# Performance work log

Hardware: AMD Instinct MI355X
Metric: run time of the kernel (lower is better)

The kernel has to match this reference:

```python
import jax, jax.numpy as jnp
import numpy as np

B, D, C = 4096, 2048, 64
L_HP, D_HP, OMEGA, EPSILON = 0.5, 1.0, 100.0, 0.1
LN_EPS = 1e-5
CLASS_COUNTS = [5000,4500,4050,3645,3280,2952,2657,2391,2152,1937,1743,1569,1412,1271,1144,1029,926,834,750,675,608,547,492,443,399,359,323,291,262,236,212,191,172,155,139,125,113,101,91,82,74,66,60,54,48,43,39,35,32,28,26,23,21,19,17,15,14,12,11,10,9,8,7,7]


def setup_inputs() -> dict:
    key = jax.random.key(0)
    k_x, k_y, k_b, k_u1, k_u2 = jax.random.split(key, 5)
    counts = jnp.asarray(CLASS_COUNTS, dtype=jnp.float32)
    # set_class_weights: tilde_C = 1/log(counts*d + eps), min-max normalized, scaled by l
    tilde = 1.0 / jnp.log(counts * D_HP + EPSILON)
    c = (tilde - jnp.min(tilde)) / (jnp.max(tilde) - jnp.min(tilde)) * L_HP
    # set_fs_classes: 1 where count <= omega
    fs_classes = jnp.where(counts <= OMEGA, 1, 0).astype(jnp.int32)
    x = jax.random.normal(k_x, (B, D), dtype=jnp.float32)
    y = jax.random.randint(k_y, (B,), 0, C)
    beta_idx = jax.random.randint(k_b, (B,), 0, B)
    u1 = jax.random.uniform(k_u1, (B,))
    u2 = jax.random.uniform(k_u2, (B,))
    alpha = jnp.where(u1 > 0.5, u2, jnp.ones((B,), jnp.float32))
    return {"x": x, "y": y, "alpha": alpha, "beta_idx": beta_idx, "c": c, "fs_classes": fs_classes}


def reference(x, y, alpha, beta_idx, c, fs_classes):
    n_batch, dim = x.shape
    num_classes = c.shape[0]
    # --- reconstruct ---
    mu = jnp.mean(x, axis=-1, keepdims=True)
    var = jnp.mean((x - mu) ** 2, axis=-1, keepdims=True)
    x_norm = (x - mu) / jnp.sqrt(var + LN_EPS) / jnp.sqrt(jnp.asarray(dim, x.dtype))
    sim = jnp.matmul(x_norm, x_norm.T)  # [B, B]
    # E[i, j] = eye[i, j] + fs_mask[j]  (broadcast over rows), thresholded to {0, 1}
    fs_mask = fs_classes[y].astype(x.dtype)  # [B]
    E = jnp.eye(n_batch, dtype=x.dtype) + fs_mask[None, :]
    E = jnp.where(E >= 1.0, 1.0, 0.0)
    sim = jax.nn.softmax(sim - 100000.0 * E, axis=-1)
    contrib = c[y]  # [B]
    reconstructions = jnp.matmul(sim, x)  # [B, D]
    R = reconstructions * contrib[:, None] + x * (1.0 - contrib)[:, None]
    # --- pairwise_mix: M @ R with M[i,:] = alpha[i]*e_i + (1-alpha[i])*e_{beta_idx[i]} ---
    y_oh = jax.nn.one_hot(y, num_classes, dtype=x.dtype)
    a = alpha[:, None]
    x_mix = a * R + (1.0 - a) * R[beta_idx]
    y_mix = a * y_oh + (1.0 - a) * y_oh[beta_idx]
    return (x_mix, y_mix)
```

## Files before the change

### kernel.cpp

```cpp
#include <hip/hip_runtime.h>
#include <cstdint>
#include <cstddef>

typedef __bf16 bf16;
typedef __bf16 bf16x8 __attribute__((ext_vector_type(8)));
typedef float floatx4 __attribute__((ext_vector_type(4)));
typedef int intx8 __attribute__((ext_vector_type(8)));

#define NB 4096
#define ND 2048
#define NCLS 64
#define TSTRIDE 144
#define OS 136

__device__ __forceinline__ void stage16(const void* g, void* l) {
  __builtin_amdgcn_global_load_lds(
      (__attribute__((address_space(1))) unsigned int*)g,
      (__attribute__((address_space(3))) unsigned int*)l, 16, 0, 0);
}

__device__ __forceinline__ unsigned char fp8x1(float f) {
  return (unsigned char)(__builtin_amdgcn_cvt_pk_fp8_f32(f, f, 0, false) & 0xFF);
}
__device__ __forceinline__ int fp8x4(float f0, float f1, float f2, float f3) {
  int d = __builtin_amdgcn_cvt_pk_fp8_f32(f0, f1, 0, false);
  return __builtin_amdgcn_cvt_pk_fp8_f32(f2, f3, d, true);
}

__device__ __forceinline__ void stage_step(const unsigned char* __restrict__ A,
                                           const unsigned char* __restrict__ B,
                                           int K, int m0, int n0, int k0,
                                           unsigned char* As,
                                           unsigned char* Bs) {
  const int t = threadIdx.x;
  const int w = t >> 6, lane = t & 63;
#pragma unroll
  for (int q = 0; q < 4; ++q) {
    const int slot = w * 256 + q * 64 + lane;
    const int row = slot >> 3;
    const int cc = (slot & 7) ^ (row & 7);
    stage16(A + (size_t)(m0 + row) * K + (k0 + cc * 16),
            As + (w * 256 + q * 64) * 16);
  }
#pragma unroll
  for (int q = 0; q < 4; ++q) {
    const int slot = w * 256 + q * 64 + lane;
    const int row = slot >> 3;
    const int cc = (slot & 7) ^ (row & 7);
    stage16(B + (size_t)(n0 + row) * K + (k0 + cc * 16),
            Bs + (w * 256 + q * 64) * 16);
  }
}

__device__ __forceinline__ void gemm_core8(const unsigned char* __restrict__ A,
                                           const unsigned char* __restrict__ B,
                                           int K, int m0, int n0,
                                           unsigned char* As0, unsigned char* Bs0,
                                           unsigned char* As1, unsigned char* Bs1,
                                           floatx4 acc[4][4]) {
  const int t = threadIdx.x;
  const int w = t >> 6;
  const int lane = t & 63;
  const int wm = w >> 1, wn = w & 1;
  const int lm = lane & 15, quad = lane >> 4;
  const int nk = K >> 7;

  stage_step(A, B, K, m0, n0, 0, As0, Bs0);

  for (int k = 0; k < nk; ++k) {
    __syncthreads();
    if (k + 1 < nk)
      stage_step(A, B, K, m0, n0, (k + 1) << 7, (k & 1) ? As0 : As1,
                 (k & 1) ? Bs0 : Bs1);
    unsigned char* Ac = (k & 1) ? As1 : As0;
    unsigned char* Bc = (k & 1) ? Bs1 : Bs0;

    intx8 af[4], bfr[4];
#pragma unroll
    for (int i = 0; i < 4; ++i) {
      const int row = wm * 64 + i * 16 + lm;
      const int c0 = (quad * 2) ^ (row & 7);
      const int4 lo = *(const int4*)(Ac + row * 128 + c0 * 16);
      const int4 hi = *(const int4*)(Ac + row * 128 + (c0 ^ 1) * 16);
      af[i][0] = lo.x; af[i][1] = lo.y; af[i][2] = lo.z; af[i][3] = lo.w;
      af[i][4] = hi.x; af[i][5] = hi.y; af[i][6] = hi.z; af[i][7] = hi.w;
    }
#pragma unroll
    for (int i = 0; i < 4; ++i) {
      const int row = wn * 64 + i * 16 + lm;
      const int c0 = (quad * 2) ^ (row & 7);
      const int4 lo = *(const int4*)(Bc + row * 128 + c0 * 16);
      const int4 hi = *(const int4*)(Bc + row * 128 + (c0 ^ 1) * 16);
      bfr[i][0] = lo.x; bfr[i][1] = lo.y; bfr[i][2] = lo.z; bfr[i][3] = lo.w;
      bfr[i][4] = hi.x; bfr[i][5] = hi.y; bfr[i][6] = hi.z; bfr[i][7] = hi.w;
    }
#pragma unroll
    for (int mi = 0; mi < 4; ++mi)
#pragma unroll
      for (int ni = 0; ni < 4; ++ni)
        acc[mi][ni] = __builtin_amdgcn_mfma_scale_f32_16x16x128_f8f6f4(
            af[mi], bfr[ni], acc[mi][ni], 0, 0, 0, 127, 0, 127);
  }
}


__global__ __launch_bounds__(256) void prep_kernel(
    const float* __restrict__ x, const int* __restrict__ y,
    const float* __restrict__ c, const int* __restrict__ fs,
    unsigned char* __restrict__ XN8, unsigned char* __restrict__ XBT8,
    float* __restrict__ lrow, float* __restrict__ contrib,
    int* __restrict__ maskcol) {
  __shared__ float tile[64][65];
  const int t = threadIdx.x;

  if (blockIdx.x < NB) {
    const int row = blockIdx.x;
    const float4* xr = (const float4*)(x + (size_t)row * ND);
    float4 v0 = xr[t], v1 = xr[t + 256];
    float s = v0.x + v0.y + v0.z + v0.w + v1.x + v1.y + v1.z + v1.w;
    float q = v0.x * v0.x + v0.y * v0.y + v0.z * v0.z + v0.w * v0.w +
              v1.x * v1.x + v1.y * v1.y + v1.z * v1.z + v1.w * v1.w;
#pragma unroll
    for (int o = 32; o > 0; o >>= 1) {
      s += __shfl_down(s, o);
      q += __shfl_down(q, o);
    }
    const int w = t >> 6;
    if ((t & 63) == 0) { tile[0][w] = s; tile[1][w] = q; }
    __syncthreads();
    s = tile[0][0] + tile[0][1] + tile[0][2] + tile[0][3];
    q = tile[1][0] + tile[1][1] + tile[1][2] + tile[1][3];
    const float mu = s * (1.0f / ND);
    const float var = q * (1.0f / ND) - mu * mu;
    const float sc =
        rsqrtf(var + 1e-5f) * 0.02209708691207961f * 32.0f;

    int* orow = (int*)(XN8 + (size_t)row * ND);
    orow[t] = fp8x4((v0.x - mu) * sc, (v0.y - mu) * sc, (v0.z - mu) * sc,
                    (v0.w - mu) * sc);
    orow[256 + t] = fp8x4((v1.x - mu) * sc, (v1.y - mu) * sc, (v1.z - mu) * sc,
                          (v1.w - mu) * sc);

    if (t == 0) {
      lrow[row] = 0.0f;
      const int yi = y[row];
      contrib[row] = c[yi];
      maskcol[row] = fs[yi];
    }
  } else {
    const int b2 = blockIdx.x - NB;
    const int rb = b2 & 63;
    const int cb = b2 >> 6;
    const int tx = t & 63, ty = t >> 6;
#pragma unroll
    for (int rr = ty; rr < 64; rr += 4)
      tile[rr][tx] = x[(size_t)(rb * 64 + rr) * ND + cb * 64 + tx];
    __syncthreads();
    const int ro = t >> 2;
    const int co = t & 3;
    int4 v;
    {
      const int j = co * 16;
      v.x = fp8x4(tile[j + 0][ro], tile[j + 1][ro], tile[j + 2][ro], tile[j + 3][ro]);
      v.y = fp8x4(tile[j + 4][ro], tile[j + 5][ro], tile[j + 6][ro], tile[j + 7][ro]);
      v.z = fp8x4(tile[j + 8][ro], tile[j + 9][ro], tile[j + 10][ro], tile[j + 11][ro]);
      v.w = fp8x4(tile[j + 12][ro], tile[j + 13][ro], tile[j + 14][ro], tile[j + 15][ro]);
    }
    *(int4*)(XBT8 + (size_t)(cb * 64 + ro) * NB + rb * 64 + co * 16) = v;
  }
}

__global__ __launch_bounds__(256) void gemm_sim_kernel(
    const unsigned char* __restrict__ XN8, unsigned char* __restrict__ P8,
    float* __restrict__ lrow, const int* __restrict__ maskcol) {
  __shared__ unsigned char smem[65536];
  unsigned char* As0 = smem;
  unsigned char* Bs0 = smem + 16384;
  unsigned char* As1 = smem + 32768;
  unsigned char* Bs1 = smem + 49152;

  const int b = blockIdx.x;
  int bj = (int)((sqrtf(8.0f * (float)b + 1.0f) - 1.0f) * 0.5f);
  while ((bj + 1) * (bj + 2) / 2 <= b) ++bj;
  while (bj * (bj + 1) / 2 > b) --bj;
  const int bi = b - bj * (bj + 1) / 2;
  const int m0 = bi * 128, n0 = bj * 128;

  floatx4 acc[4][4];
#pragma unroll
  for (int i = 0; i < 4; ++i)
#pragma unroll
    for (int j = 0; j < 4; ++j) acc[i][j] = 0.0f;

  gemm_core8(XN8, XN8, ND, m0, n0, As0, Bs0, As1, Bs1, acc);

  const int t = threadIdx.x, w = t >> 6, lane = t & 63;
  const int wm = w >> 1, wn = w & 1, lm = lane & 15, quad = lane >> 4;

  int cmj[4];
#pragma unroll
  for (int ni = 0; ni < 4; ++ni) cmj[ni] = maskcol[n0 + wn * 64 + ni * 16 + lm];
  int rmk[4][4];
#pragma unroll
  for (int mi = 0; mi < 4; ++mi)
#pragma unroll
    for (int r = 0; r < 4; ++r)
      rmk[mi][r] = maskcol[m0 + wm * 64 + mi * 16 + quad * 4 + r];

  float rs[4][4];
#pragma unroll
  for (int mi = 0; mi < 4; ++mi)
#pragma unroll
    for (int r = 0; r < 4; ++r) rs[mi][r] = 0.0f;

#pragma unroll
  for (int ni = 0; ni < 4; ++ni) {
    const int gcol = n0 + wn * 64 + ni * 16 + lm;
#pragma unroll
    for (int mi = 0; mi < 4; ++mi) {
#pragma unroll
      for (int r = 0; r < 4; ++r) {
        const int grow = m0 + wm * 64 + mi * 16 + quad * 4 + r;
        float e = (grow == gcol) ? 0.0f
                                 : __expf(acc[mi][ni][r] * 0.0009765625f);
        acc[mi][ni][r] = e;
        rs[mi][r] += cmj[ni] ? 0.0f : e;
      }
    }
  }
#pragma unroll
  for (int mi = 0; mi < 4; ++mi)
#pragma unroll
    for (int r = 0; r < 4; ++r) {
      float vsum = rs[mi][r];
      vsum += __shfl_xor(vsum, 1);
      vsum += __shfl_xor(vsum, 2);
      vsum += __shfl_xor(vsum, 4);
      vsum += __shfl_xor(vsum, 8);
      if (lm == 0)
        atomicAdd(&lrow[m0 + wm * 64 + mi * 16 + quad * 4 + r], vsum);
    }

  __syncthreads();
#pragma unroll
  for (int ni = 0; ni < 4; ++ni) {
    const int col = wn * 64 + ni * 16 + lm;
#pragma unroll
    for (int mi = 0; mi < 4; ++mi)
#pragma unroll
      for (int r = 0; r < 4; ++r) {
        const int row = wm * 64 + mi * 16 + quad * 4 + r;
        smem[row * TSTRIDE + col] = fp8x1(cmj[ni] ? 0.0f : acc[mi][ni][r]);
      }
  }
  __syncthreads();
#pragma unroll
  for (int it = 0; it < 4; ++it) {
    const int row = it * 32 + (t >> 3), ch = t & 7;
    int4 v = *(const int4*)(smem + row * TSTRIDE + ch * 16);
    *(int4*)(P8 + (size_t)(m0 + row) * NB + n0 + ch * 16) = v;
  }

  if (bi != bj) {
    __syncthreads();
#pragma unroll
    for (int ni = 0; ni < 4; ++ni) {
      const int tc = wn * 64 + ni * 16 + lm;
      float cs = 0.0f;
#pragma unroll
      for (int mi = 0; mi < 4; ++mi) {
        float g0 = rmk[mi][0] ? 0.0f : acc[mi][ni][0];
        float g1 = rmk[mi][1] ? 0.0f : acc[mi][ni][1];
        float g2 = rmk[mi][2] ? 0.0f : acc[mi][ni][2];
        float g3 = rmk[mi][3] ? 0.0f : acc[mi][ni][3];
        cs += g0 + g1 + g2 + g3;
        *(int*)(smem + tc * TSTRIDE + wm * 64 + mi * 16 + quad * 4) =
            fp8x4(g0, g1, g2, g3);
      }
      cs += __shfl_xor(cs, 16);
      cs += __shfl_xor(cs, 32);
      if (quad == 0) atomicAdd(&lrow[n0 + tc], cs);
    }
    __syncthreads();
#pragma unroll
    for (int it = 0; it < 4; ++it) {
      const int row = it * 32 + (t >> 3), ch = t & 7;
      int4 v = *(const int4*)(smem + row * TSTRIDE + ch * 16);
      *(int4*)(P8 + (size_t)(n0 + row) * NB + m0 + ch * 16) = v;
    }
  }
}

__global__ __launch_bounds__(256) void gemm_recon_kernel(
    const unsigned char* __restrict__ P8, const unsigned char* __restrict__ XBT8,
    const float* __restrict__ x, const float* __restrict__ lrow,
    const float* __restrict__ contrib, bf16* __restrict__ R) {
  __shared__ unsigned char smem[65536];
  unsigned char* As0 = smem;
  unsigned char* Bs0 = smem + 16384;
  unsigned char* As1 = smem + 32768;
  unsigned char* Bs1 = smem + 49152;

  const int id = blockIdx.x;
  const int xcd = id & 7;
  const int s = id >> 3;
  const int bx = xcd * 2 + (s & 1);
  const int by = s >> 1;
  const int m0 = by * 128, n0 = bx * 128;

  floatx4 acc[4][4];
#pragma unroll
  for (int i = 0; i < 4; ++i)
#pragma unroll
    for (int j = 0; j < 4; ++j) acc[i][j] = 0.0f;

  gemm_core8(P8, XBT8, NB, m0, n0, As0, Bs0, As1, Bs1, acc);

  const int t = threadIdx.x, w = t >> 6, lane = t & 63;
  const int wm = w >> 1, wn = w & 1, lm = lane & 15, quad = lane >> 4;

  __syncthreads();
  bf16* osm = (bf16*)smem;
#pragma unroll
  for (int mi = 0; mi < 4; ++mi) {
#pragma unroll
    for (int r = 0; r < 4; ++r) {
      const int lrow_i = wm * 64 + mi * 16 + quad * 4 + r;
      const int grow = m0 + lrow_i;
      const float inv = 1.0f / lrow[grow];
      const float ci = contrib[grow];
#pragma unroll
      for (int ni = 0; ni < 4; ++ni) {
        const int lcol = wn * 64 + ni * 16 + lm;
        const float rec = acc[mi][ni][r] * inv;
        const float xv = x[(size_t)grow * ND + n0 + lcol];
        osm[lrow_i * OS + lcol] = (bf16)(rec * ci + xv * (1.0f - ci));
      }
    }
  }
  __syncthreads();
#pragma unroll
  for (int it = 0; it < 8; ++it) {
    const int row = it * 16 + (t >> 4), ch = t & 15;
    int4 v = *(const int4*)(osm + row * OS + ch * 8);
    *(int4*)(R + (size_t)(m0 + row) * ND + n0 + ch * 8) = v;
  }
}

__global__ __launch_bounds__(256) void mix_kernel(
    const bf16* __restrict__ R, const float* __restrict__ alpha,
    const int* __restrict__ beta_idx, const int* __restrict__ y,
    float* __restrict__ out) {
  const int i = blockIdx.x, t = threadIdx.x;
  const float a = alpha[i];
  const int bi = beta_idx[i];
  const bf16x8* Ri = (const bf16x8*)(R + (size_t)i * ND);
  const bf16x8* Rb = (const bf16x8*)(R + (size_t)bi * ND);
  const float b = 1.0f - a;
  bf16x8 r = Ri[t], g = Rb[t];
  float4 o0, o1;
  o0.x = a * (float)r[0] + b * (float)g[0];
  o0.y = a * (float)r[1] + b * (float)g[1];
  o0.z = a * (float)r[2] + b * (float)g[2];
  o0.w = a * (float)r[3] + b * (float)g[3];
  o1.x = a * (float)r[4] + b * (float)g[4];
  o1.y = a * (float)r[5] + b * (float)g[5];
  o1.z = a * (float)r[6] + b * (float)g[6];
  o1.w = a * (float)r[7] + b * (float)g[7];
  float4* o = (float4*)(out + (size_t)i * ND + t * 8);
  o[0] = o0;
  o[1] = o1;
  if (t < NCLS) {
    const int yi = y[i], yb = y[bi];
    const float v = a * (t == yi ? 1.0f : 0.0f) + b * (t == yb ? 1.0f : 0.0f);
    out[(size_t)NB * ND + (size_t)i * NCLS + t] = v;
  }
}

extern "C" void kernel_launch(void* const* d_in, const int* in_sizes, int n_in,
                              void* d_out, int out_size, void* d_ws,
                              size_t ws_size, hipStream_t stream) {
  const float* x = (const float*)d_in[0];
  const int* y = (const int*)d_in[1];
  const float* alpha = (const float*)d_in[2];
  const int* beta = (const int*)d_in[3];
  const float* c = (const float*)d_in[4];
  const int* fs = (const int*)d_in[5];
  float* out = (float*)d_out;
  char* ws = (char*)d_ws;

  unsigned char* XN8  = (unsigned char*)(ws + 0);
  unsigned char* XBT8 = (unsigned char*)(ws + 8388608);
  unsigned char* P8   = (unsigned char*)(ws + 16777216);
  bf16* R   = (bf16*)(ws + 33554432);
  float* LR = (float*)(ws + 50331648);
  float* CT = (float*)(ws + 50331648 + 16384);
  int* MC   = (int*)(ws + 50331648 + 32768);

  prep_kernel<<<NB + 2048, 256, 0, stream>>>(x, y, c, fs, XN8, XBT8, LR, CT, MC);
  gemm_sim_kernel<<<528, 256, 0, stream>>>(XN8, P8, LR, MC);
  gemm_recon_kernel<<<512, 256, 0, stream>>>(P8, XBT8, x, LR, CT, R);
  mix_kernel<<<NB, 256, 0, stream>>>(R, alpha, beta, y, out);
}
```

Before: 179.1 us.

## Interleave LDS reads with MFMAs, stage bf16 copy of x, move label mix to prep

Replaces the read-all-then-compute inner loop of the fp8 GEMM core with a hand-ordered sequence that interleaves LDS fragment reads with MFMA issues, so LDS latency overlaps matrix math. Prep now also writes a bf16 copy of x, which the recon epilogue reads instead of fp32 x, halving that epilogue's read traffic at the cost of extra writes in prep and a small precision loss on the residual term. The one-hot label mixing moves from mix_kernel into extra prep blocks.

```diff
diff --git a/kernel.cpp b/kernel.cpp
--- a/kernel.cpp
+++ b/kernel.cpp
@@ -3,6 +3,7 @@
 #include <cstddef>
 
 typedef __bf16 bf16;
+typedef __bf16 bf16x4 __attribute__((ext_vector_type(4)));
 typedef __bf16 bf16x8 __attribute__((ext_vector_type(8)));
 typedef float floatx4 __attribute__((ext_vector_type(4)));
 typedef int intx8 __attribute__((ext_vector_type(8)));
@@ -51,6 +52,28 @@
             Bs + (w * 256 + q * 64) * 16);
   }
 }
+
+#define READ_A(i)                                                       \
+  {                                                                     \
+    const int row = wm * 64 + (i)*16 + lm;                              \
+    const int c0 = (quad * 2) ^ (row & 7);                              \
+    const int4 lo = *(const int4*)(Ac + row * 128 + c0 * 16);           \
+    const int4 hi = *(const int4*)(Ac + row * 128 + (c0 ^ 1) * 16);     \
+    af[i][0] = lo.x; af[i][1] = lo.y; af[i][2] = lo.z; af[i][3] = lo.w; \
+    af[i][4] = hi.x; af[i][5] = hi.y; af[i][6] = hi.z; af[i][7] = hi.w; \
+  }
+#define READ_B(i)                                                            \
+  {                                                                          \
+    const int row = wn * 64 + (i)*16 + lm;                                   \
+    const int c0 = (quad * 2) ^ (row & 7);                                   \
+    const int4 lo = *(const int4*)(Bc + row * 128 + c0 * 16);                \
+    const int4 hi = *(const int4*)(Bc + row * 128 + (c0 ^ 1) * 16);          \
+    bfr[i][0] = lo.x; bfr[i][1] = lo.y; bfr[i][2] = lo.z; bfr[i][3] = lo.w;  \
+    bfr[i][4] = hi.x; bfr[i][5] = hi.y; bfr[i][6] = hi.z; bfr[i][7] = hi.w;  \
+  }
+#define MFMA(mi, ni)                                                \
+  acc[mi][ni] = __builtin_amdgcn_mfma_scale_f32_16x16x128_f8f6f4(   \
+      af[mi], bfr[ni], acc[mi][ni], 0, 0, 0, 127, 0, 127)
 
 __device__ __forceinline__ void gemm_core8(const unsigned char* __restrict__ A,
                                            const unsigned char* __restrict__ B,
@@ -76,40 +99,25 @@
     unsigned char* Bc = (k & 1) ? Bs1 : Bs0;
 
     intx8 af[4], bfr[4];
-#pragma unroll
-    for (int i = 0; i < 4; ++i) {
-      const int row = wm * 64 + i * 16 + lm;
-      const int c0 = (quad * 2) ^ (row & 7);
-      const int4 lo = *(const int4*)(Ac + row * 128 + c0 * 16);
-      const int4 hi = *(const int4*)(Ac + row * 128 + (c0 ^ 1) * 16);
-      af[i][0] = lo.x; af[i][1] = lo.y; af[i][2] = lo.z; af[i][3] = lo.w;
-      af[i][4] = hi.x; af[i][5] = hi.y; af[i][6] = hi.z; af[i][7] = hi.w;
-    }
-#pragma unroll
-    for (int i = 0; i < 4; ++i) {
-      const int row = wn * 64 + i * 16 + lm;
-      const int c0 = (quad * 2) ^ (row & 7);
-      const int4 lo = *(const int4*)(Bc + row * 128 + c0 * 16);
-      const int4 hi = *(const int4*)(Bc + row * 128 + (c0 ^ 1) * 16);
-      bfr[i][0] = lo.x; bfr[i][1] = lo.y; bfr[i][2] = lo.z; bfr[i][3] = lo.w;
-      bfr[i][4] = hi.x; bfr[i][5] = hi.y; bfr[i][6] = hi.z; bfr[i][7] = hi.w;
-    }
-#pragma unroll
-    for (int mi = 0; mi < 4; ++mi)
-#pragma unroll
-      for (int ni = 0; ni < 4; ++ni)
-        acc[mi][ni] = __builtin_amdgcn_mfma_scale_f32_16x16x128_f8f6f4(
-            af[mi], bfr[ni], acc[mi][ni], 0, 0, 0, 127, 0, 127);
+    READ_A(0); READ_A(1); READ_B(0); READ_B(1);
+    MFMA(0, 0); MFMA(0, 1); MFMA(1, 0); MFMA(1, 1);
+    READ_A(2); READ_A(3);
+    MFMA(2, 0); MFMA(2, 1); MFMA(3, 0); MFMA(3, 1);
+    READ_B(2); READ_B(3);
+    MFMA(0, 2); MFMA(0, 3); MFMA(1, 2); MFMA(1, 3);
+    MFMA(2, 2); MFMA(2, 3); MFMA(3, 2); MFMA(3, 3);
   }
 }
 
 
 __global__ __launch_bounds__(256) void prep_kernel(
     const float* __restrict__ x, const int* __restrict__ y,
+    const float* __restrict__ alpha, const int* __restrict__ beta_idx,
     const float* __restrict__ c, const int* __restrict__ fs,
     unsigned char* __restrict__ XN8, unsigned char* __restrict__ XBT8,
-    float* __restrict__ lrow, float* __restrict__ contrib,
-    int* __restrict__ maskcol) {
+    bf16* __restrict__ XB16, float* __restrict__ lrow,
+    float* __restrict__ contrib, int* __restrict__ maskcol,
+    float* __restrict__ out) {
   __shared__ float tile[64][65];
   const int t = threadIdx.x;
 
@@ -141,13 +149,19 @@
     orow[256 + t] = fp8x4((v1.x - mu) * sc, (v1.y - mu) * sc, (v1.z - mu) * sc,
                           (v1.w - mu) * sc);
 
+    bf16x4 b0, b1;
+    b0[0] = (bf16)v0.x; b0[1] = (bf16)v0.y; b0[2] = (bf16)v0.z; b0[3] = (bf16)v0.w;
+    b1[0] = (bf16)v1.x; b1[1] = (bf16)v1.y; b1[2] = (bf16)v1.z; b1[3] = (bf16)v1.w;
+    *(bf16x4*)(XB16 + (size_t)row * ND + t * 4) = b0;
+    *(bf16x4*)(XB16 + (size_t)row * ND + 1024 + t * 4) = b1;
+
     if (t == 0) {
       lrow[row] = 0.0f;
       const int yi = y[row];
       contrib[row] = c[yi];
       maskcol[row] = fs[yi];
     }
-  } else {
+  } else if (blockIdx.x < NB + 2048) {
     const int b2 = blockIdx.x - NB;
     const int rb = b2 & 63;
     const int cb = b2 >> 6;
@@ -167,6 +181,15 @@
       v.w = fp8x4(tile[j + 12][ro], tile[j + 13][ro], tile[j + 14][ro], tile[j + 15][ro]);
     }
     *(int4*)(XBT8 + (size_t)(cb * 64 + ro) * NB + rb * 64 + co * 16) = v;
+  } else {
+    const int b3 = blockIdx.x - (NB + 2048);
+    const int row = b3 * 4 + (t >> 6);
+    const int cls = t & 63;
+    const float a = alpha[row];
+    const int bi = beta_idx[row];
+    const int yi = y[row], yb = y[bi];
+    out[(size_t)NB * ND + (size_t)row * NCLS + cls] =
+        a * (cls == yi ? 1.0f : 0.0f) + (1.0f - a) * (cls == yb ? 1.0f : 0.0f);
   }
 }
 
@@ -293,7 +316,7 @@
 
 __global__ __launch_bounds__(256) void gemm_recon_kernel(
     const unsigned char* __restrict__ P8, const unsigned char* __restrict__ XBT8,
-    const float* __restrict__ x, const float* __restrict__ lrow,
+    const bf16* __restrict__ XB16, const float* __restrict__ lrow,
     const float* __restrict__ contrib, bf16* __restrict__ R) {
   __shared__ unsigned char smem[65536];
   unsigned char* As0 = smem;
@@ -333,7 +356,7 @@
       for (int ni = 0; ni < 4; ++ni) {
         const int lcol = wn * 64 + ni * 16 + lm;
         const float rec = acc[mi][ni][r] * inv;
-        const float xv = x[(size_t)grow * ND + n0 + lcol];
+        const float xv = (float)XB16[(size_t)grow * ND + n0 + lcol];
         osm[lrow_i * OS + lcol] = (bf16)(rec * ci + xv * (1.0f - ci));
       }
     }
@@ -349,8 +372,7 @@
 
 __global__ __launch_bounds__(256) void mix_kernel(
     const bf16* __restrict__ R, const float* __restrict__ alpha,
-    const int* __restrict__ beta_idx, const int* __restrict__ y,
-    float* __restrict__ out) {
+    const int* __restrict__ beta_idx, float* __restrict__ out) {
   const int i = blockIdx.x, t = threadIdx.x;
   const float a = alpha[i];
   const int bi = beta_idx[i];
@@ -370,11 +392,6 @@
   float4* o = (float4*)(out + (size_t)i * ND + t * 8);
   o[0] = o0;
   o[1] = o1;
-  if (t < NCLS) {
-    const int yi = y[i], yb = y[bi];
-    const float v = a * (t == yi ? 1.0f : 0.0f) + b * (t == yb ? 1.0f : 0.0f);
-    out[(size_t)NB * ND + (size_t)i * NCLS + t] = v;
-  }
 }
 
 extern "C" void kernel_launch(void* const* d_in, const int* in_sizes, int n_in,
@@ -392,13 +409,16 @@
   unsigned char* XN8  = (unsigned char*)(ws + 0);
   unsigned char* XBT8 = (unsigned char*)(ws + 8388608);
   unsigned char* P8   = (unsigned char*)(ws + 16777216);
-  bf16* R   = (bf16*)(ws + 33554432);
-  float* LR = (float*)(ws + 50331648);
-  float* CT = (float*)(ws + 50331648 + 16384);
-  int* MC   = (int*)(ws + 50331648 + 32768);
-
-  prep_kernel<<<NB + 2048, 256, 0, stream>>>(x, y, c, fs, XN8, XBT8, LR, CT, MC);
+  bf16* R    = (bf16*)(ws + 33554432);
+  bf16* XB16 = (bf16*)(ws + 50331648);
+  float* LR = (float*)(ws + 67108864);
+  float* CT = (float*)(ws + 67108864 + 16384);
+  int* MC   = (int*)(ws + 67108864 + 32768);
+
+  prep_kernel<<<NB + 2048 + 1024, 256, 0, stream>>>(x, y, alpha, beta, c, fs,
+                                                    XN8, XBT8, XB16, LR, CT,
+                                                    MC, out);
   gemm_sim_kernel<<<528, 256, 0, stream>>>(XN8, P8, LR, MC);
-  gemm_recon_kernel<<<512, 256, 0, stream>>>(P8, XBT8, x, LR, CT, R);
-  mix_kernel<<<NB, 256, 0, stream>>>(R, alpha, beta, y, out);
-}
+  gemm_recon_kernel<<<512, 256, 0, stream>>>(P8, XBT8, XB16, LR, CT, R);
+  mix_kernel<<<NB, 256, 0, stream>>>(R, alpha, beta, out);
+}
```

After: 180.1 us. No clear change (+0.6%).
